# Performance work log

Hardware: AMD Instinct MI355X
Metric: run time of the kernel (lower is better)

Reference implementation:

```python
import jax, jax.numpy as jnp
import numpy as np
from jax import lax

B, N = 4096, 2048  # batteries, Euler steps (throughput has N+1 columns)
D_IN, D_HID = 5, 10


def setup_inputs() -> dict:
    key = jax.random.key(0)
    ks = jax.random.split(key, 10)
    # monotone throughput so Euler step sizes h are positive and realistic
    thr = jnp.cumsum(jax.random.uniform(ks[0], (B, N + 1), jnp.float32) * 0.01, axis=1)
    return {
        "throughput": thr,
        "DOD": jax.random.uniform(ks[1], (1, B), jnp.float32),
        "V_av": jax.random.uniform(ks[2], (1, B), jnp.float32) * 0.8 + 3.2,
        "C_0": jax.random.uniform(ks[3], (1, B), jnp.float32) * 0.2 + 0.9,
        "R_0": jax.random.uniform(ks[4], (1, B), jnp.float32) * 0.05 + 0.01,
        "W1": jax.random.normal(ks[5], (D_HID, D_IN), jnp.float32) / np.sqrt(D_IN),
        "b1": jax.random.normal(ks[6], (D_HID,), jnp.float32) * 0.01,
        "W2": jax.random.normal(ks[7], (D_IN, D_HID), jnp.float32) / np.sqrt(D_HID),
        "b2": jax.random.normal(ks[8], (D_IN,), jnp.float32) * 0.01,
        "n": N,
    }


def reference(throughput, DOD, V_av, C_0, R_0, W1, b1, W2, b2, n):
    # initial state per battery: [thr_0, DOD, V_av, C_0, R_0] -> [B, 5]
    init = jnp.concatenate(
        [throughput[:, 0:1], DOD.T, V_av.T, C_0.T, R_0.T], axis=1
    )

    def f(y):  # tiny MLP: Linear(5,10)-Tanh-Linear(10,5)
        return jnp.tanh(y @ W1.T + b1) @ W2.T + b2

    thr_next = throughput[:, 1 : n + 1]              # [B, n]
    hs = thr_next - throughput[:, 0:n]               # [B, n] Euler step sizes

    def step(state, xs):
        h, t = xs                                    # each [B]
        y_new = state + h[:, None] * f(state)        # Euler step on full state
        # pin feature 0 to current throughput, reset features 1:3 to initial
        new_state = jnp.concatenate(
            [t[:, None], state[:, 1:3], y_new[:, 3:5]], axis=1
        )
        return new_state, new_state[:, 3:5]

    _, outs = lax.scan(step, init, (hs.T, thr_next.T))  # outs: [n, B, 2]
    traj = jnp.concatenate([init[None, :, 3:5], outs], axis=0)  # [n+1, B, 2]
    return jnp.transpose(traj, (1, 0, 2))            # [B, n+1, 2]
```

## Files before the change

kernel.cpp:

```cpp
#include <hip/hip_runtime.h>

typedef float v2f __attribute__((ext_vector_type(2)));

__device__ __forceinline__ float scan64(float d) {
    d += __int_as_float(__builtin_amdgcn_update_dpp(0, __float_as_int(d), 0x111, 0xF, 0xF, true));
    d += __int_as_float(__builtin_amdgcn_update_dpp(0, __float_as_int(d), 0x112, 0xF, 0xF, true));
    d += __int_as_float(__builtin_amdgcn_update_dpp(0, __float_as_int(d), 0x114, 0xF, 0xF, true));
    d += __int_as_float(__builtin_amdgcn_update_dpp(0, __float_as_int(d), 0x118, 0xF, 0xF, true));
    d += __int_as_float(__builtin_amdgcn_update_dpp(0, __float_as_int(d), 0x142, 0xA, 0xF, true));
    d += __int_as_float(__builtin_amdgcn_update_dpp(0, __float_as_int(d), 0x143, 0xC, 0xF, true));
    return d;
}

__device__ __forceinline__ float rdl63(float v) {
    return __int_as_float(__builtin_amdgcn_readlane(__float_as_int(v), 63));
}

__global__ __launch_bounds__(64, 4) void ode_wf256x4(
    const float* __restrict__ thr,
    const float* __restrict__ DOD,
    const float* __restrict__ Vav,
    const float* __restrict__ C0,
    const float* __restrict__ R0,
    const float* __restrict__ W1,
    const float* __restrict__ b1,
    const float* __restrict__ W2,
    const float* __restrict__ b2,
    float* __restrict__ out,
    int B, int N)
{
    const int j   = threadIdx.x & 63;
    const int row = blockIdx.x;
    if (row >= B) return;

    const float k2  = 2.0f * 1.4426950408889634f;
    const float ln2 = 0.6931471805599453f;
    const float dod = DOD[row], vav = Vav[row];

    v2f bw[5], w0k[5], w3k[5], w4k[5], wa[5], wb[5];
    float c3 = b2[3], c4 = b2[4];
#pragma unroll
    for (int i = 0; i < 5; ++i) {
#pragma unroll
        for (int p = 0; p < 2; ++p) {
            int h = i + 5 * p;
            float a0 = W1[h * 5 + 0];
            float a1 = W1[h * 5 + 1];
            float a2 = W1[h * 5 + 2];
            float a3 = W1[h * 5 + 3];
            float a4 = W1[h * 5 + 4];
            bw[i][p]  = k2 * (b1[h] + a1 * dod + a2 * vav);
            w0k[i][p] = k2 * a0;
            w3k[i][p] = k2 * a3;
            w4k[i][p] = k2 * a4;
            float v3 = W2[30 + h];
            float v4 = W2[40 + h];
            c3 += v3; c4 += v4;
            wa[i][p] = -2.0f * v3;
            wb[i][p] = -2.0f * v4;
        }
    }

    float Y3 = C0[row], Y4 = R0[row];
    const float* trp = thr + (size_t)row * (size_t)(N + 1);
    float2* orow = (float2*)(out + (size_t)row * (size_t)(N + 1) * 2);
    if (j == 0) orow[0] = make_float2(Y3, Y4);

    float t[5];
#pragma unroll
    for (int k = 0; k < 5; ++k) t[k] = trp[min(4 * j + k, N)];
    float tb = trp[0];

    float F3p, F4p;
    {
        v2f Fa = {c3, 0.f}, Fb = {c4, 0.f};
#pragma unroll
        for (int i = 0; i < 5; ++i) {
            v2f x = w3k[i] * Y3 + (w4k[i] * Y4 + (w0k[i] * tb + bw[i]));
            v2f e; e.x = __builtin_amdgcn_exp2f(x.x); e.y = __builtin_amdgcn_exp2f(x.y);
            v2f A = e + 1.0f;
            v2f s; s.x = __builtin_amdgcn_rcpf(A.x); s.y = __builtin_amdgcn_rcpf(A.y);
            Fa += wa[i] * s;
            Fb += wb[i] * s;
        }
        F3p = Fa.x + Fa.y; F4p = Fb.x + Fb.y;
    }
    float dF3 = 0.f, dF4 = 0.f;

    const int nblk = (N + 255) >> 8;
    const int gInt = max(0, N / 256 - 1);

    for (int g = 0; g < nblk; ++g) {
        const int base = g << 8;
        const int nb = base + 256;

        float pt[5], ptb;
        if (g < gInt) {
#pragma unroll
            for (int k = 0; k < 5; ++k) pt[k] = trp[nb + 4 * j + k];
            ptb = trp[nb];
        } else {
#pragma unroll
            for (int k = 0; k < 5; ++k) pt[k] = trp[min(nb + 4 * j + k, N)];
            ptb = trp[min(nb, N)];
        }

        const float h0 = t[1] - t[0];
        const float h1 = t[2] - t[1];
        const float h2 = t[3] - t[2];
        const float h3 = t[4] - t[3];

        float z3[4], z4[4];
#pragma unroll
        for (int k = 0; k < 4; ++k) {
            float dt = t[k] - tb;
            z3[k] = fmaf(dt, fmaf(0.5f * dt, dF3, F3p), Y3);
            z4[k] = fmaf(dt, fmaf(0.5f * dt, dF4, F4p), Y4);
        }

        v2f tq[5];
        float F30, F40;
        {
            v2f Fa = {c3, 0.f}, Fb = {c4, 0.f};
#pragma unroll
            for (int i = 0; i < 5; ++i) {
                v2f x = w3k[i] * z3[0] + (w4k[i] * z4[0] + (w0k[i] * t[0] + bw[i]));
                v2f e; e.x = __builtin_amdgcn_exp2f(x.x);
                       e.y = __builtin_amdgcn_exp2f(x.y);
                v2f A = e + 1.0f;
                v2f s; s.x = __builtin_amdgcn_rcpf(A.x);
                       s.y = __builtin_amdgcn_rcpf(A.y);
                tq[i] = s;
                Fa += wa[i] * s;
                Fb += wb[i] * s;
            }
            F30 = Fa.x + Fa.y; F40 = Fb.x + Fb.y;
        }
#pragma unroll
        for (int i = 0; i < 5; ++i) tq[i] = tq[i] - tq[i] * tq[i];

        float K3a, K4a, Kta, K3b, K4b, Ktb;
        {
            v2f a3 = {0.f,0.f}, a4 = {0.f,0.f}, at = {0.f,0.f};
            v2f b3 = {0.f,0.f}, b4 = {0.f,0.f}, bt = {0.f,0.f};
#pragma unroll
            for (int i = 0; i < 5; ++i) {
                v2f ma = wa[i] * tq[i];
                v2f mb = wb[i] * tq[i];
                a3 += ma * w3k[i]; a4 += ma * w4k[i]; at += ma * w0k[i];
                b3 += mb * w3k[i]; b4 += mb * w4k[i]; bt += mb * w0k[i];
            }
            K3a = ln2 * (a3.x + a3.y); K4a = ln2 * (a4.x + a4.y);
            Kta = ln2 * (at.x + at.y);
            K3b = ln2 * (b3.x + b3.y); K4b = ln2 * (b4.x + b4.y);
            Ktb = ln2 * (bt.x + bt.y);
        }

        float F3v[4], F4v[4];
        F3v[0] = F30; F4v[0] = F40;
#pragma unroll
        for (int k = 1; k < 4; ++k) {
            float D3 = z3[k] - z3[0];
            float D4 = z4[k] - z4[0];
            float Dt = t[k] - t[0];
            F3v[k] = F30 - fmaf(K3a, D3, fmaf(K4a, D4, Kta * Dt));
            F4v[k] = F40 - fmaf(K3b, D3, fmaf(K4b, D4, Ktb * Dt));
        }

        float d3 = fmaf(h0, F3v[0], fmaf(h1, F3v[1], fmaf(h2, F3v[2], h3 * F3v[3])));
        float d4 = fmaf(h0, F4v[0], fmaf(h1, F4v[1], fmaf(h2, F4v[2], h3 * F4v[3])));
        float S3 = scan64(d3);
        float S4 = scan64(d4);

        float dm3, dm4;
        {
            float cc3 = Y3 + (S3 - d3), cc4 = Y4 + (S4 - d4);
            dm3 = h0 * (cc3 - z3[0]);  dm4 = h0 * (cc4 - z4[0]);
            cc3 = fmaf(h0, F3v[0], cc3); cc4 = fmaf(h0, F4v[0], cc4);
            dm3 = fmaf(h1, cc3 - z3[1], dm3); dm4 = fmaf(h1, cc4 - z4[1], dm4);
            cc3 = fmaf(h1, F3v[1], cc3); cc4 = fmaf(h1, F4v[1], cc4);
            dm3 = fmaf(h2, cc3 - z3[2], dm3); dm4 = fmaf(h2, cc4 - z4[2], dm4);
            cc3 = fmaf(h2, F3v[2], cc3); cc4 = fmaf(h2, F4v[2], cc4);
            dm3 = fmaf(h3, cc3 - z3[3], dm3); dm4 = fmaf(h3, cc4 - z4[3], dm4);
        }

        float d3p = d3 - fmaf(K3a, dm3, K4a * dm4);
        float d4p = d4 - fmaf(K3b, dm3, K4b * dm4);
        float S3p = scan64(d3p);
        float S4p = scan64(d4p);

        float o3 = Y3 + S3p, o4 = Y4 + S4p;
        const int p0 = base + 4 * j;
        if (p0 + 3 < N) orow[p0 + 4] = make_float2(o3, o4);
        float q3 = fmaf(-h3, F3v[3], o3), q4 = fmaf(-h3, F4v[3], o4);
        if (p0 + 2 < N) orow[p0 + 3] = make_float2(q3, q4);
        q3 = fmaf(-h2, F3v[2], q3); q4 = fmaf(-h2, F4v[2], q4);
        if (p0 + 1 < N) orow[p0 + 2] = make_float2(q3, q4);
        q3 = fmaf(-h1, F3v[1], q3); q4 = fmaf(-h1, F4v[1], q4);
        if (p0 < N)     orow[p0 + 1] = make_float2(q3, q4);

        float F3n = rdl63(F3v[3]);
        float F4n = rdl63(F4v[3]);
        Y3 += rdl63(S3p);
        Y4 += rdl63(S4p);
        float span = ptb - tb;
        float inv = (span > 0.f) ? __builtin_amdgcn_rcpf(span) : 0.f;
        dF3 = (F3n - F3p) * inv;
        dF4 = (F4n - F4p) * inv;
        F3p = F3n; F4p = F4n;

#pragma unroll
        for (int k = 0; k < 5; ++k) t[k] = pt[k];
        tb = ptb;
    }
}

extern "C" void kernel_launch(void* const* d_in, const int* in_sizes, int n_in,
                              void* d_out, int out_size, void* d_ws, size_t ws_size,
                              hipStream_t stream) {
    const float* thr = (const float*)d_in[0];
    const float* DOD = (const float*)d_in[1];
    const float* Vav = (const float*)d_in[2];
    const float* C0  = (const float*)d_in[3];
    const float* R0  = (const float*)d_in[4];
    const float* W1  = (const float*)d_in[5];
    const float* b1  = (const float*)d_in[6];
    const float* W2  = (const float*)d_in[7];
    const float* b2  = (const float*)d_in[8];
    float* out = (float*)d_out;

    int B = in_sizes[1];
    int N = in_sizes[0] / B - 1;

    dim3 block(64);
    dim3 grid(B);
    ode_wf256x4<<<grid, block, 0, stream>>>(thr, DOD, Vav, C0, R0,
                                            W1, b1, W2, b2, out, B, N);
}
```

Baseline: 33.85 us.

## Prefetch throughput two blocks ahead and flatten correction accumulation chain

Throughput values are now loaded two 256-step blocks ahead using a three-stage register rotation (current, next, far), which hides more global load latency behind each block's compute. The serial cc/dm accumulation in the correction pass is rewritten as prefix sums plus independent error terms combined in a tree, which shortens the dependency chain. The cost is extra registers for the second prefetch buffer, and the reassociated sums change rounding slightly. The fast path that skipped clamping for interior blocks is removed, so every load is now clamped.

After: 33.96 us. No clear change (+0.3%).

```diff
diff --git a/kernel.cpp b/kernel.cpp
--- a/kernel.cpp
+++ b/kernel.cpp
@@ -16,7 +16,7 @@
     return __int_as_float(__builtin_amdgcn_readlane(__float_as_int(v), 63));
 }
 
-__global__ __launch_bounds__(64, 4) void ode_wf256x4(
+__global__ __launch_bounds__(64, 4) void ode_wf256x4d2(
     const float* __restrict__ thr,
     const float* __restrict__ DOD,
     const float* __restrict__ Vav,
@@ -66,17 +66,20 @@
     float2* orow = (float2*)(out + (size_t)row * (size_t)(N + 1) * 2);
     if (j == 0) orow[0] = make_float2(Y3, Y4);
 
-    float t[5];
-#pragma unroll
-    for (int k = 0; k < 5; ++k) t[k] = trp[min(4 * j + k, N)];
-    float tb = trp[0];
+    float tc[5], tn[5], tbc, tbn;
+#pragma unroll
+    for (int k = 0; k < 5; ++k) tc[k] = trp[min(4 * j + k, N)];
+    tbc = trp[0];
+#pragma unroll
+    for (int k = 0; k < 5; ++k) tn[k] = trp[min(256 + 4 * j + k, N)];
+    tbn = trp[min(256, N)];
 
     float F3p, F4p;
     {
         v2f Fa = {c3, 0.f}, Fb = {c4, 0.f};
 #pragma unroll
         for (int i = 0; i < 5; ++i) {
-            v2f x = w3k[i] * Y3 + (w4k[i] * Y4 + (w0k[i] * tb + bw[i]));
+            v2f x = w3k[i] * Y3 + (w4k[i] * Y4 + (w0k[i] * tbc + bw[i]));
             v2f e; e.x = __builtin_amdgcn_exp2f(x.x); e.y = __builtin_amdgcn_exp2f(x.y);
             v2f A = e + 1.0f;
             v2f s; s.x = __builtin_amdgcn_rcpf(A.x); s.y = __builtin_amdgcn_rcpf(A.y);
@@ -88,32 +91,25 @@
     float dF3 = 0.f, dF4 = 0.f;
 
     const int nblk = (N + 255) >> 8;
-    const int gInt = max(0, N / 256 - 1);
 
     for (int g = 0; g < nblk; ++g) {
         const int base = g << 8;
-        const int nb = base + 256;
-
-        float pt[5], ptb;
-        if (g < gInt) {
-#pragma unroll
-            for (int k = 0; k < 5; ++k) pt[k] = trp[nb + 4 * j + k];
-            ptb = trp[nb];
-        } else {
-#pragma unroll
-            for (int k = 0; k < 5; ++k) pt[k] = trp[min(nb + 4 * j + k, N)];
-            ptb = trp[min(nb, N)];
-        }
-
-        const float h0 = t[1] - t[0];
-        const float h1 = t[2] - t[1];
-        const float h2 = t[3] - t[2];
-        const float h3 = t[4] - t[3];
+
+        const int pf = base + 512;
+        float tf[5], tbf;
+#pragma unroll
+        for (int k = 0; k < 5; ++k) tf[k] = trp[min(pf + 4 * j + k, N)];
+        tbf = trp[min(pf, N)];
+
+        const float h0 = tc[1] - tc[0];
+        const float h1 = tc[2] - tc[1];
+        const float h2 = tc[3] - tc[2];
+        const float h3 = tc[4] - tc[3];
 
         float z3[4], z4[4];
 #pragma unroll
         for (int k = 0; k < 4; ++k) {
-            float dt = t[k] - tb;
+            float dt = tc[k] - tbc;
             z3[k] = fmaf(dt, fmaf(0.5f * dt, dF3, F3p), Y3);
             z4[k] = fmaf(dt, fmaf(0.5f * dt, dF4, F4p), Y4);
         }
@@ -124,7 +120,7 @@
             v2f Fa = {c3, 0.f}, Fb = {c4, 0.f};
 #pragma unroll
             for (int i = 0; i < 5; ++i) {
-                v2f x = w3k[i] * z3[0] + (w4k[i] * z4[0] + (w0k[i] * t[0] + bw[i]));
+                v2f x = w3k[i] * z3[0] + (w4k[i] * z4[0] + (w0k[i] * tc[0] + bw[i]));
                 v2f e; e.x = __builtin_amdgcn_exp2f(x.x);
                        e.y = __builtin_amdgcn_exp2f(x.y);
                 v2f A = e + 1.0f;
@@ -162,7 +158,7 @@
         for (int k = 1; k < 4; ++k) {
             float D3 = z3[k] - z3[0];
             float D4 = z4[k] - z4[0];
-            float Dt = t[k] - t[0];
+            float Dt = tc[k] - tc[0];
             F3v[k] = F30 - fmaf(K3a, D3, fmaf(K4a, D4, Kta * Dt));
             F4v[k] = F40 - fmaf(K3b, D3, fmaf(K4b, D4, Ktb * Dt));
         }
@@ -174,14 +170,23 @@
 
         float dm3, dm4;
         {
-            float cc3 = Y3 + (S3 - d3), cc4 = Y4 + (S4 - d4);
-            dm3 = h0 * (cc3 - z3[0]);  dm4 = h0 * (cc4 - z4[0]);
-            cc3 = fmaf(h0, F3v[0], cc3); cc4 = fmaf(h0, F4v[0], cc4);
-            dm3 = fmaf(h1, cc3 - z3[1], dm3); dm4 = fmaf(h1, cc4 - z4[1], dm4);
-            cc3 = fmaf(h1, F3v[1], cc3); cc4 = fmaf(h1, F4v[1], cc4);
-            dm3 = fmaf(h2, cc3 - z3[2], dm3); dm4 = fmaf(h2, cc4 - z4[2], dm4);
-            cc3 = fmaf(h2, F3v[2], cc3); cc4 = fmaf(h2, F4v[2], cc4);
-            dm3 = fmaf(h3, cc3 - z3[3], dm3); dm4 = fmaf(h3, cc4 - z4[3], dm4);
+            float cb3 = Y3 + (S3 - d3), cb4 = Y4 + (S4 - d4);
+            float a1 = h0 * F3v[0];
+            float a2 = fmaf(h1, F3v[1], a1);
+            float a3 = fmaf(h2, F3v[2], a2);
+            float b1_ = h0 * F4v[0];
+            float b2_ = fmaf(h1, F4v[1], b1_);
+            float b3_ = fmaf(h2, F4v[2], b2_);
+            float e0 = cb3 - z3[0];
+            float e1 = (cb3 + a1) - z3[1];
+            float e2 = (cb3 + a2) - z3[2];
+            float e3 = (cb3 + a3) - z3[3];
+            dm3 = fmaf(h0, e0, h1 * e1) + fmaf(h2, e2, h3 * e3);
+            float f0 = cb4 - z4[0];
+            float f1 = (cb4 + b1_) - z4[1];
+            float f2 = (cb4 + b2_) - z4[2];
+            float f3 = (cb4 + b3_) - z4[3];
+            dm4 = fmaf(h0, f0, h1 * f1) + fmaf(h2, f2, h3 * f3);
         }
 
         float d3p = d3 - fmaf(K3a, dm3, K4a * dm4);
@@ -203,15 +208,15 @@
         float F4n = rdl63(F4v[3]);
         Y3 += rdl63(S3p);
         Y4 += rdl63(S4p);
-        float span = ptb - tb;
+        float span = tbn - tbc;
         float inv = (span > 0.f) ? __builtin_amdgcn_rcpf(span) : 0.f;
         dF3 = (F3n - F3p) * inv;
         dF4 = (F4n - F4p) * inv;
         F3p = F3n; F4p = F4n;
 
 #pragma unroll
-        for (int k = 0; k < 5; ++k) t[k] = pt[k];
-        tb = ptb;
+        for (int k = 0; k < 5; ++k) { tc[k] = tn[k]; tn[k] = tf[k]; }
+        tbc = tbn; tbn = tbf;
     }
 }
 
@@ -234,6 +239,6 @@
 
     dim3 block(64);
     dim3 grid(B);
-    ode_wf256x4<<<grid, block, 0, stream>>>(thr, DOD, Vav, C0, R0,
-                                            W1, b1, W2, b2, out, B, N);
-}
+    ode_wf256x4d2<<<grid, block, 0, stream>>>(thr, DOD, Vav, C0, R0,
+                                              W1, b1, W2, b2, out, B, N);
+}
```
